# Kernel optimization log

Hardware: AMD Instinct MI355X
Metric: run time of the kernel (lower is better)

The kernel has to match this reference:

```python
import jax, jax.numpy as jnp
import numpy as np

V, E, D_LAT, NC, L = 30000, 256, 256, 10, 4096
B = 8
D_IN = 2 * D_LAT   # mamba expand=2 -> 512
N_ST = 16          # d_state
DT_R = 16          # dt_rank = ceil(d_model/16)
D_CONV = 4


def conv1d(x, w, b, pad, groups=1):
    # x: [B,C,L], w: [O, C//groups, K] (torch layout)
    y = jax.lax.conv_general_dilated(x, w, (1,), [(pad[0], pad[1])],
                                     dimension_numbers=('NCH', 'OIH', 'NCH'),
                                     feature_group_count=groups)
    return y + b[None, :, None]


def setup_inputs() -> dict:
    key = jax.random.key(0)
    ks = jax.random.split(key, 12)
    nrm = lambda k, s, sc=0.02: (jax.random.normal(k, s) * sc).astype(jnp.float32)
    return {
        'tokens': jax.random.randint(ks[0], (B, L), 0, V),
        'emb': nrm(ks[1], (V, E)),
        'conv1_w': nrm(ks[2], (128, E, 5)), 'conv1_b': jnp.zeros((128,), jnp.float32),
        'conv2_w': nrm(ks[3], (D_LAT, 128, 3)), 'conv2_b': jnp.zeros((D_LAT,), jnp.float32),
        'in_proj_w': nrm(ks[4], (2 * D_IN, D_LAT)),
        'convdw_w': nrm(ks[5], (D_IN, 1, D_CONV), 0.2), 'convdw_b': jnp.zeros((D_IN,), jnp.float32),
        'x_proj_w': nrm(ks[6], (DT_R + 2 * N_ST, D_IN)),
        'dt_proj_w': nrm(ks[7], (D_IN, DT_R), 0.1),
        'dt_proj_b': jnp.full((D_IN,), -4.0, jnp.float32),  # softplus^-1 of small dt
        'A_log': jnp.broadcast_to(jnp.log(jnp.arange(1, N_ST + 1, dtype=jnp.float32)), (D_IN, N_ST)) + jnp.zeros((D_IN, N_ST), jnp.float32),
        'Dp': jnp.ones((D_IN,), jnp.float32),
        'out_proj_w': nrm(ks[8], (D_LAT, D_IN)),
        'fc_w': nrm(ks[9], (NC, D_LAT)), 'fc_b': jnp.zeros((NC,), jnp.float32),
    }


def mamba_block(u, in_proj_w, convdw_w, convdw_b, x_proj_w, dt_proj_w, dt_proj_b, A_log, Dp, out_proj_w):
    # u: [B, Lm, d_model]
    Bsz = u.shape[0]
    xz = u @ in_proj_w.T                              # [B,Lm,2*Din]
    x, z = jnp.split(xz, 2, axis=-1)
    # causal depthwise conv (torch pads both sides, slices [:L] == left-pad only)
    xc = conv1d(x.transpose(0, 2, 1), convdw_w, convdw_b, (D_CONV - 1, 0), groups=D_IN)
    x = jax.nn.silu(xc.transpose(0, 2, 1))            # [B,Lm,Din]
    dbc = x @ x_proj_w.T                              # [B,Lm,dt_rank+2N]
    dt, Bm, Cm = jnp.split(dbc, [DT_R, DT_R + N_ST], axis=-1)
    dt = jax.nn.softplus(dt @ dt_proj_w.T + dt_proj_b)  # [B,Lm,Din]
    A = -jnp.exp(A_log)                               # [Din,N]

    def step(h, inp):
        dt_t, B_t, C_t, x_t = inp                     # [B,Din],[B,N],[B,N],[B,Din]
        dA = jnp.exp(dt_t[..., None] * A)             # [B,Din,N]
        h = h * dA + (dt_t * x_t)[..., None] * B_t[:, None, :]
        y = jnp.einsum('bdn,bn->bd', h, C_t)
        return h, y

    h0 = jnp.zeros((Bsz, D_IN, N_ST), u.dtype)
    xs = (dt.transpose(1, 0, 2), Bm.transpose(1, 0, 2), Cm.transpose(1, 0, 2), x.transpose(1, 0, 2))
    _, ys = jax.lax.scan(step, h0, xs)                # [Lm,B,Din]
    y = ys.transpose(1, 0, 2) + x * Dp
    y = y * jax.nn.silu(z)
    return y @ out_proj_w.T                           # [B,Lm,d_model]


def reference(tokens, emb, conv1_w, conv1_b, conv2_w, conv2_b, in_proj_w, convdw_w, convdw_b,
              x_proj_w, dt_proj_w, dt_proj_b, A_log, Dp, out_proj_w, fc_w, fc_b):
    x = emb[tokens]                                   # [B,L,E]
    x = x.transpose(0, 2, 1)                          # [B,E,L]
    x = jax.nn.relu(conv1d(x, conv1_w, conv1_b, (2, 2)))
    b, c, l = x.shape
    x = x.reshape(b, c, l // 2, 2).max(-1)            # MaxPool1d(2)
    x = jax.nn.relu(conv1d(x, conv2_w, conv2_b, (1, 1)))
    x = x.transpose(0, 2, 1)                          # [B,L/2,latent]
    x = mamba_block(x, in_proj_w, convdw_w, convdw_b, x_proj_w, dt_proj_w, dt_proj_b, A_log, Dp, out_proj_w)
    x = x.mean(axis=1)                                # [B,latent]
    return x @ fc_w.T + fc_b                          # [B,num_classes]
```

## Files before the change

### kernel.cpp

```cpp
#include <hip/hip_runtime.h>
#include <hip/hip_bf16.h>

constexpr int Bn   = 8;
constexpr int L    = 4096;
constexpr int E    = 256;
constexpr int Lh   = 2048;
constexpr int C1n  = 128;
constexpr int Dlat = 256;
constexpr int Din  = 512;
constexpr int Nst  = 16;
constexpr int M2   = Bn * Lh;
constexpr int NCH  = 64;
constexpr int TC   = 32;

constexpr long o_wtx   = 0;
constexpr long o_wtdt  = o_wtx  + 512L*48;
constexpr long o_bf    = o_wtdt + 16L*512;
constexpr long o_xeb   = o_bf    + 524288/2;
constexpr long o_out1b = o_xeb   + (8L*4100*256)/2;
constexpr long o_ub    = o_out1b + (8L*2050*128)/2;
constexpr long o_xz    = o_ub    + (16384L*256)/2;
constexpr long o_xbuf  = o_xz    + 16384L*1024;
constexpr long o_dbc   = o_xbuf  + 16384L*512;
constexpr long o_dt    = o_dbc   + 16384L*48;
constexpr long o_hend  = o_dt    + 16384L*512;
constexpr long o_P     = o_hend  + 8L*512*NCH*16;
constexpr long o_hin   = o_P     + 8L*512*NCH*16;
constexpr long o_ym    = o_hin   + 8L*512*NCH*16;
constexpr long o_S     = o_ym    + 8L*512;
constexpr long o_yp    = o_S     + 8L*512*NCH*16;

typedef __attribute__((ext_vector_type(8))) short bf8_t;
typedef __attribute__((ext_vector_type(4))) float f4_t;

__device__ inline short f2bf(float f) {
    unsigned int u = __float_as_uint(f);
    unsigned int r = (u + 0x7FFFu + ((u >> 16) & 1u)) >> 16;
    return (short)r;
}

__global__ void k_prep(const float* __restrict__ w1, const float* __restrict__ w2,
                       const float* __restrict__ win, const float* __restrict__ xw,
                       const float* __restrict__ dtw, float* __restrict__ ws) {
    int idx = blockIdx.x * 256 + threadIdx.x;
    if (idx < 24576) {
        int n_ = idx % 48; int k = idx / 48;
        ws[o_wtx + idx] = xw[n_*512 + k];
    } else if (idx < 32768) {
        int j = idx - 24576;
        int n_ = j & 511; int k = j >> 9;
        ws[o_wtdt + j] = dtw[n_*16 + k];
    } else if (idx < 557056) {
        int j = idx - 32768;
        short* wsS = (short*)(ws + o_bf);
        if (j < 163840) {
            int n_ = j / 1280; int r = j - n_*1280; int s = r >> 8; int c = r & 255;
            wsS[j] = f2bf(w1[(n_*256 + c)*5 + s]);
        } else if (j < 262144) {
            int jj = j - 163840;
            int n_ = jj / 384; int r = jj - n_*384; int s = r >> 7; int c = r & 127;
            wsS[j] = f2bf(w2[(n_*128 + c)*3 + s]);
        } else {
            int jj = j - 262144;
            int n_ = jj >> 8; int k = jj & 255;
            wsS[j] = f2bf(win[n_*256 + k]);
        }
    }
}

__global__ void k_embed(const int* __restrict__ tok, const float* __restrict__ emb,
                        short* __restrict__ xeb) {
    int idx = blockIdx.x * 256 + threadIdx.x;
    int r = idx >> 5;
    int c8 = (idx & 31) << 3;
    int b = r / 4100; int tr = r - b*4100;
    bf8_t v = {0,0,0,0,0,0,0,0};
    if (tr >= 2 && tr < 4098) {
        int t = tok[b*4096 + tr - 2];
        const float* e = emb + (long)t*256 + c8;
        #pragma unroll
        for (int i = 0; i < 8; ++i) v[i] = f2bf(e[i]);
    }
    *(bf8_t*)&xeb[(long)r*256 + c8] = v;
}

__global__ void k_zpad(short* __restrict__ out1b) {
    int i = threadIdx.x;
    for (int j = i; j < 2048; j += 256) {
        int b = j >> 8; int rsel = (j >> 7) & 1; int c = j & 127;
        long row = (long)b*2050 + (rsel ? 2049 : 0);
        out1b[row*128 + c] = 0;
    }
}

template<int SHIFTS, int TPS, int EPI>
__global__ __launch_bounds__(256) void k_mgemm(const short* __restrict__ A, int ars, long batchA,
                                               const short* __restrict__ Bt, int ktot,
                                               const float* __restrict__ bias,
                                               short* __restrict__ outB, float* __restrict__ outF,
                                               int ors, long batchOut) {
    constexpr int KT = SHIFTS * TPS;
    constexpr int C  = TPS * 64;
    __shared__ short As[2][64][68];
    __shared__ short Bs[2][128][68];
    int tid = threadIdx.x;
    int l = tid & 63, w = tid >> 6;
    int m0 = blockIdx.x * 64;
    int n0 = blockIdx.y * 128;
    long zA = (long)blockIdx.z * batchA;
    long zO = (long)blockIdx.z * batchOut;

    bf8_t aReg[2], bReg[4];

    auto gload = [&](int kt) {
        int s = kt / TPS, c0 = (kt % TPS) * 64;
        const short* Ab = A + zA + (long)(m0 + s) * ars + c0;
        #pragma unroll
        for (int j = 0; j < 2; ++j) {
            int idx = tid + j*256;
            int r = idx >> 3, cc = (idx & 7) * 8;
            aReg[j] = *(const bf8_t*)&Ab[(long)r * ars + cc];
        }
        const short* Bb = Bt + (long)n0 * ktot + s * C + c0;
        #pragma unroll
        for (int j = 0; j < 4; ++j) {
            int idx = tid + j*256;
            int r = idx >> 3, cc = (idx & 7) * 8;
            bReg[j] = *(const bf8_t*)&Bb[(long)r * ktot + cc];
        }
    };
    auto lwrite = [&](int buf) {
        #pragma unroll
        for (int j = 0; j < 2; ++j) {
            int idx = tid + j*256;
            int r = idx >> 3, cc = (idx & 7) * 8;
            *(bf8_t*)&As[buf][r][cc] = aReg[j];
        }
        #pragma unroll
        for (int j = 0; j < 4; ++j) {
            int idx = tid + j*256;
            int r = idx >> 3, cc = (idx & 7) * 8;
            *(bf8_t*)&Bs[buf][r][cc] = bReg[j];
        }
    };

    f4_t acc[4][2];
    #pragma unroll
    for (int m = 0; m < 4; ++m)
        #pragma unroll
        for (int n = 0; n < 2; ++n) acc[m][n] = (f4_t){0.f, 0.f, 0.f, 0.f};

    gload(0);
    lwrite(0);
    __syncthreads();
    for (int kt = 0; kt < KT; ++kt) {
        int buf = kt & 1;
        if (kt + 1 < KT) gload(kt + 1);
        #pragma unroll
        for (int ks = 0; ks < 2; ++ks) {
            int kk = ks*32 + ((l >> 4) << 3);
            bf8_t a[4], b[2];
            #pragma unroll
            for (int m = 0; m < 4; ++m)
                a[m] = *(const bf8_t*)&As[buf][m*16 + (l & 15)][kk];
            #pragma unroll
            for (int n = 0; n < 2; ++n)
                b[n] = *(const bf8_t*)&Bs[buf][w*32 + n*16 + (l & 15)][kk];
            #pragma unroll
            for (int m = 0; m < 4; ++m)
                #pragma unroll
                for (int n = 0; n < 2; ++n)
                    acc[m][n] = __builtin_amdgcn_mfma_f32_16x16x32_bf16(a[m], b[n], acc[m][n], 0, 0, 0);
        }
        if (kt + 1 < KT) {
            lwrite(buf ^ 1);
            __syncthreads();
        }
    }

    #pragma unroll
    for (int mt = 0; mt < 4; ++mt)
        #pragma unroll
        for (int nt = 0; nt < 2; ++nt) {
            f4_t c = acc[mt][nt];
            int col = n0 + w*32 + nt*16 + (l & 15);
            int r0 = m0 + mt*16 + ((l >> 4) << 2);
            if constexpr (EPI == 0) {
                #pragma unroll
                for (int j = 0; j < 4; ++j)
                    outF[zO + (long)(r0 + j) * ors + col] = c[j];
            } else if constexpr (EPI == 1) {
                float bv = bias[col];
                #pragma unroll
                for (int j = 0; j < 4; ++j)
                    outB[zO + (long)(r0 + j) * ors + col] = f2bf(fmaxf(c[j] + bv, 0.f));
            } else {
                float bv = bias[col];
                float p0 = fmaxf(fmaxf(c[0], c[1]) + bv, 0.f);
                float p1 = fmaxf(fmaxf(c[2], c[3]) + bv, 0.f);
                int tp = r0 >> 1;
                outB[zO + (long)(tp + 1) * ors + col] = f2bf(p0);
                outB[zO + (long)(tp + 2) * ors + col] = f2bf(p1);
            }
        }
}

template<int ACT>
__global__ __launch_bounds__(256) void k_gemm(const float* __restrict__ A, int lda,
                                              const float* __restrict__ WT,
                                              const float* __restrict__ bias,
                                              float* __restrict__ out,
                                              int M, int N, int K) {
    __shared__ float As[16][68];
    __shared__ float Bs[16][64];
    int n0 = blockIdx.x * 64, m0 = blockIdx.y * 64;
    int tid = threadIdx.x;
    int ti = tid >> 4, tj = tid & 15;
    float acc[4][4] = {};
    for (int k0 = 0; k0 < K; k0 += 16) {
        {
            int mm = tid >> 2, kq = tid & 3;
            float4 v = *(const float4*)&A[(long)(m0 + mm)*lda + k0 + kq*4];
            As[kq*4+0][mm] = v.x; As[kq*4+1][mm] = v.y;
            As[kq*4+2][mm] = v.z; As[kq*4+3][mm] = v.w;
        }
        {
            int kk = tid >> 4, n4 = tid & 15;
            float4 v = {0.f,0.f,0.f,0.f};
            if (n0 + n4*4 < N)
                v = *(const float4*)&WT[(long)(k0 + kk)*N + n0 + n4*4];
            *(float4*)&Bs[kk][n4*4] = v;
        }
        __syncthreads();
        #pragma unroll
        for (int kk = 0; kk < 16; ++kk) {
            float4 av = *(float4*)&As[kk][ti*4];
            float4 bv = *(float4*)&Bs[kk][tj*4];
            acc[0][0] += av.x*bv.x; acc[0][1] += av.x*bv.y; acc[0][2] += av.x*bv.z; acc[0][3] += av.x*bv.w;
            acc[1][0] += av.y*bv.x; acc[1][1] += av.y*bv.y; acc[1][2] += av.y*bv.z; acc[1][3] += av.y*bv.w;
            acc[2][0] += av.z*bv.x; acc[2][1] += av.z*bv.y; acc[2][2] += av.z*bv.z; acc[2][3] += av.z*bv.w;
            acc[3][0] += av.w*bv.x; acc[3][1] += av.w*bv.y; acc[3][2] += av.w*bv.z; acc[3][3] += av.w*bv.w;
        }
        __syncthreads();
    }
    if (n0 + tj*4 >= N) return;
    float4 bv = {0.f,0.f,0.f,0.f};
    if (bias) bv = *(const float4*)&bias[n0 + tj*4];
    #pragma unroll
    for (int i = 0; i < 4; ++i) {
        int m = m0 + ti*4 + i;
        float4 v;
        v.x = acc[i][0] + bv.x; v.y = acc[i][1] + bv.y;
        v.z = acc[i][2] + bv.z; v.w = acc[i][3] + bv.w;
        if (ACT == 1) {
            v.x = (v.x > 20.f) ? v.x : log1pf(__expf(v.x));
            v.y = (v.y > 20.f) ? v.y : log1pf(__expf(v.y));
            v.z = (v.z > 20.f) ? v.z : log1pf(__expf(v.z));
            v.w = (v.w > 20.f) ? v.w : log1pf(__expf(v.w));
        }
        *(float4*)&out[(long)m*N + n0 + tj*4] = v;
    }
}

__global__ __launch_bounds__(256) void k_dwconv(const float* __restrict__ xz,
                                                const float* __restrict__ wdw,
                                                const float* __restrict__ bdw,
                                                float* __restrict__ xout) {
    __shared__ float wk[4][512];
    __shared__ float bs[512];
    int tid = threadIdx.x;
    for (int e = tid; e < 2048; e += 256) {
        int k = e >> 9, d = e & 511;
        wk[k][d] = wdw[d*4 + k];
    }
    bs[tid] = bdw[tid];
    bs[tid + 256] = bdw[tid + 256];
    __syncthreads();

    int idx = blockIdx.x * 256 + tid;
    int d4 = idx & 127;
    int tg = (idx >> 7) & 511;
    int b  = idx >> 16;
    int d0 = d4 * 4;
    int t0 = tg * 4;

    float4 x[7];
    #pragma unroll
    for (int i = 0; i < 7; ++i) {
        int t = t0 - 3 + i;
        x[i] = (t >= 0) ? *(const float4*)&xz[((long)(b*Lh + t))*1024 + d0]
                        : (float4){0.f, 0.f, 0.f, 0.f};
    }
    float4 w[4];
    #pragma unroll
    for (int k = 0; k < 4; ++k) w[k] = *(float4*)&wk[k][d0];
    float4 bias4 = *(float4*)&bs[d0];

    #pragma unroll
    for (int j = 0; j < 4; ++j) {
        float4 a = bias4;
        #pragma unroll
        for (int k = 0; k < 4; ++k) {
            float4 v = x[j + k];
            a.x += v.x * w[k].x; a.y += v.y * w[k].y;
            a.z += v.z * w[k].z; a.w += v.w * w[k].w;
        }
        a.x = a.x / (1.f + __expf(-a.x));
        a.y = a.y / (1.f + __expf(-a.y));
        a.z = a.z / (1.f + __expf(-a.z));
        a.w = a.w / (1.f + __expf(-a.w));
        *(float4*)&xout[((long)(b*Lh + t0 + j))*512 + d0] = a;
    }
}

__global__ __launch_bounds__(256) void k_scan_a(const float* __restrict__ dt,
                                                const float* __restrict__ x,
                                                const float* __restrict__ xz,
                                                const float* __restrict__ dbc,
                                                const float* __restrict__ A_log,
                                                const float* __restrict__ Dp,
                                                float* __restrict__ hend,
                                                float* __restrict__ Pbuf,
                                                float* __restrict__ Sbuf,
                                                float* __restrict__ ypart) {
    __shared__ float4 Bs4[TC][4], Cs4[TC][4];
    int c = blockIdx.x;
    int b = blockIdx.z;
    int tid = threadIdx.x;
    int d = blockIdx.y * 256 + tid;
    for (int i = tid; i < TC*4; i += 256) {
        int tt = i >> 2, q = i & 3;
        long rb = ((long)b*Lh + c*TC + tt)*48;
        Bs4[tt][q] = *(const float4*)&dbc[rb + 16 + q*4];
        Cs4[tt][q] = *(const float4*)&dbc[rb + 32 + q*4];
    }
    __syncthreads();
    float A_[16];
    #pragma unroll
    for (int n = 0; n < 16; ++n) A_[n] = -__expf(A_log[d*16 + n]);
    float h[16], q[16], S[16];
    #pragma unroll
    for (int n = 0; n < 16; ++n) { h[n] = 0.f; q[n] = 1.f; S[n] = 0.f; }
    float Dpv = Dp[d];
    float yp = 0.f;
    long base  = ((long)b*Lh + c*TC)*512 + d;
    long zbase = ((long)b*Lh + c*TC)*1024 + 512 + d;
    for (int tt = 0; tt < TC; ++tt) {
        float dtv = dt[base + (long)tt*512];
        float xv  = x[base + (long)tt*512];
        float zv  = xz[zbase + (long)tt*1024];
        float u = dtv * xv;
        float gate = zv / (1.f + __expf(-zv));
        float Bv[16], Cv[16];
        *(float4*)&Bv[0]  = Bs4[tt][0]; *(float4*)&Bv[4]  = Bs4[tt][1];
        *(float4*)&Bv[8]  = Bs4[tt][2]; *(float4*)&Bv[12] = Bs4[tt][3];
        *(float4*)&Cv[0]  = Cs4[tt][0]; *(float4*)&Cv[4]  = Cs4[tt][1];
        *(float4*)&Cv[8]  = Cs4[tt][2]; *(float4*)&Cv[12] = Cs4[tt][3];
        float p = 0.f;
        #pragma unroll
        for (int n = 0; n < 16; ++n) {
            float dA = __expf(dtv * A_[n]);
            h[n] = h[n] * dA + u * Bv[n];
            q[n] *= dA;
            p += h[n] * Cv[n];
            S[n] += (gate * Cv[n]) * q[n];
        }
        yp += gate * (p + xv * Dpv);
    }
    long o = (((long)b*Din + d)*NCH + c)*16;
    #pragma unroll
    for (int n = 0; n < 16; ++n) hend[o + n] = h[n];
    #pragma unroll
    for (int n = 0; n < 16; ++n) Pbuf[o + n] = q[n];
    #pragma unroll
    for (int n = 0; n < 16; ++n) Sbuf[o + n] = S[n];
    ypart[((long)b*Din + d)*NCH + c] = yp;
}

__global__ void k_scan_b(const float* __restrict__ hend, const float* __restrict__ Pbuf,
                         float* __restrict__ hin) {
    int idx = blockIdx.x * 256 + threadIdx.x;
    int n = idx & 15; long bd = idx >> 4;
    long base = bd * NCH * 16 + n;
    float h = 0.f;
    for (int c = 0; c < NCH; ++c) {
        hin[base + c*16] = h;
        h = hend[base + c*16] + Pbuf[base + c*16] * h;
    }
}

__global__ __launch_bounds__(256) void k_scan_cl(const float* __restrict__ Sbuf,
                                                 const float* __restrict__ hin,
                                                 const float* __restrict__ ypart,
                                                 float* __restrict__ ym) {
    int idx = blockIdx.x * 256 + threadIdx.x;
    int c = idx & 63;
    long bd = idx >> 6;
    long o = (bd * NCH + c) * 16;
    float v = ypart[bd * NCH + c];
    #pragma unroll
    for (int qq = 0; qq < 4; ++qq) {
        float4 s = *(const float4*)&Sbuf[o + qq*4];
        float4 hi = *(const float4*)&hin[o + qq*4];
        v += s.x*hi.x + s.y*hi.y + s.z*hi.z + s.w*hi.w;
    }
    v += __shfl_xor(v, 1);
    v += __shfl_xor(v, 2);
    v += __shfl_xor(v, 4);
    v += __shfl_xor(v, 8);
    v += __shfl_xor(v, 16);
    v += __shfl_xor(v, 32);
    if (c == 0) ym[bd] = v;
}

__global__ void k_tail(const float* __restrict__ ym, const float* __restrict__ ow,
                       const float* __restrict__ fcw, const float* __restrict__ fcb,
                       float* __restrict__ out) {
    __shared__ float yls[512];
    __shared__ float xs[256];
    int b = blockIdx.x, c = threadIdx.x;
    yls[c] = ym[b*512 + c];
    yls[c + 256] = ym[b*512 + 256 + c];
    __syncthreads();
    float s = 0.f;
    for (int d = 0; d < 512; ++d) s += yls[d] * ow[c*512 + d];
    xs[c] = s * (1.f / 2048.f);
    __syncthreads();
    if (c < 10) {
        float t = fcb[c];
        for (int k = 0; k < 256; ++k) t += xs[k] * fcw[c*256 + k];
        out[b*10 + c] = t;
    }
}

extern "C" void kernel_launch(void* const* d_in, const int* in_sizes, int n_in,
                              void* d_out, int out_size, void* d_ws, size_t ws_size,
                              hipStream_t stream) {
    const int*   tok  = (const int*)d_in[0];
    const float* emb  = (const float*)d_in[1];
    const float* w1   = (const float*)d_in[2];
    const float* b1   = (const float*)d_in[3];
    const float* w2   = (const float*)d_in[4];
    const float* b2   = (const float*)d_in[5];
    const float* win  = (const float*)d_in[6];
    const float* wdw  = (const float*)d_in[7];
    const float* bdw  = (const float*)d_in[8];
    const float* xw   = (const float*)d_in[9];
    const float* dtw  = (const float*)d_in[10];
    const float* dtb  = (const float*)d_in[11];
    const float* alog = (const float*)d_in[12];
    const float* Dp   = (const float*)d_in[13];
    const float* ow   = (const float*)d_in[14];
    const float* fcw  = (const float*)d_in[15];
    const float* fcb  = (const float*)d_in[16];
    float* ws  = (float*)d_ws;
    float* out = (float*)d_out;

    float* wtx   = ws + o_wtx;
    float* wtdt  = ws + o_wtdt;
    short* wt1t  = (short*)(ws + o_bf);
    short* wt2t  = wt1t + 163840;
    short* wtint = wt2t + 98304;
    short* xeb   = (short*)(ws + o_xeb);
    short* out1b = (short*)(ws + o_out1b);
    short* ub    = (short*)(ws + o_ub);
    float* xz    = ws + o_xz;
    float* xbuf  = ws + o_xbuf;
    float* dbc   = ws + o_dbc;
    float* dtbuf = ws + o_dt;
    float* hend  = ws + o_hend;
    float* Pbuf  = ws + o_P;
    float* hin   = ws + o_hin;
    float* ym    = ws + o_ym;
    float* Sbuf  = ws + o_S;
    float* ypart = ws + o_yp;

    k_prep<<<2176, 256, 0, stream>>>(w1, w2, win, xw, dtw, ws);
    k_embed<<<4100, 256, 0, stream>>>(tok, emb, xeb);
    k_zpad<<<1, 256, 0, stream>>>(out1b);
    k_mgemm<5, 4, 2><<<dim3(64, 1, 8), 256, 0, stream>>>(
        xeb, 256, 4100L*256, wt1t, 1280, b1, out1b, nullptr, 128, 2050L*128);
    k_mgemm<3, 2, 1><<<dim3(32, 2, 8), 256, 0, stream>>>(
        out1b, 128, 2050L*128, wt2t, 384, b2, ub, nullptr, 256, 2048L*256);
    k_mgemm<1, 4, 0><<<dim3(256, 8, 1), 256, 0, stream>>>(
        ub, 256, 0, wtint, 256, nullptr, nullptr, xz, 1024, 0);
    k_dwconv<<<2048, 256, 0, stream>>>(xz, wdw, bdw, xbuf);
    k_gemm<0><<<dim3(1, M2/64), 256, 0, stream>>>(xbuf, Din, wtx, nullptr, dbc, M2, 48, Din);
    k_gemm<1><<<dim3(8, M2/64), 256, 0, stream>>>(dbc, 48, wtdt, dtb, dtbuf, M2, 512, 16);
    k_scan_a<<<dim3(NCH, 2, Bn), 256, 0, stream>>>(dtbuf, xbuf, xz, dbc, alog, Dp,
                                                   hend, Pbuf, Sbuf, ypart);
    k_scan_b<<<(Bn*Din*Nst)/256, 256, 0, stream>>>(hend, Pbuf, hin);
    k_scan_cl<<<(Bn*Din*NCH)/256, 256, 0, stream>>>(Sbuf, hin, ypart, ym);
    k_tail<<<8, 256, 0, stream>>>(ym, ow, fcw, fcb, out);
}
```

Before: 353.9 us.

## Fuse dt projection into scan, merge chunk-combine kernels, halve scan chunk length

Drops the separate dt_proj GEMM and its dt buffer. Each scan thread now computes dt from the 16 dt-rank values staged in shared memory, its own dt_proj weights, and softplus. The inter-chunk state recurrence and the S·h_in reduction are merged into one kernel, so the h_in buffer is no longer needed. Chunk count doubles to 128 with 16 steps each, which gives the scan more parallelism but makes the sequential combine loop and the chunk buffers twice as long.

```diff
diff --git a/kernel.cpp b/kernel.cpp
--- a/kernel.cpp
+++ b/kernel.cpp
@@ -10,8 +10,8 @@
 constexpr int Din  = 512;
 constexpr int Nst  = 16;
 constexpr int M2   = Bn * Lh;
-constexpr int NCH  = 64;
-constexpr int TC   = 32;
+constexpr int NCH  = 128;
+constexpr int TC   = 16;
 
 constexpr long o_wtx   = 0;
 constexpr long o_wtdt  = o_wtx  + 512L*48;
@@ -22,13 +22,11 @@
 constexpr long o_xz    = o_ub    + (16384L*256)/2;
 constexpr long o_xbuf  = o_xz    + 16384L*1024;
 constexpr long o_dbc   = o_xbuf  + 16384L*512;
-constexpr long o_dt    = o_dbc   + 16384L*48;
-constexpr long o_hend  = o_dt    + 16384L*512;
+constexpr long o_hend  = o_dbc   + 16384L*48;
 constexpr long o_P     = o_hend  + 8L*512*NCH*16;
-constexpr long o_hin   = o_P     + 8L*512*NCH*16;
-constexpr long o_ym    = o_hin   + 8L*512*NCH*16;
-constexpr long o_S     = o_ym    + 8L*512;
-constexpr long o_yp    = o_S     + 8L*512*NCH*16;
+constexpr long o_S     = o_P     + 8L*512*NCH*16;
+constexpr long o_ym    = o_S     + 8L*512*NCH*16;
+constexpr long o_yp    = o_ym    + 8L*512;
 
 typedef __attribute__((ext_vector_type(8))) short bf8_t;
 typedef __attribute__((ext_vector_type(4))) float f4_t;
@@ -313,31 +311,36 @@
     }
 }
 
-__global__ __launch_bounds__(256) void k_scan_a(const float* __restrict__ dt,
-                                                const float* __restrict__ x,
+__global__ __launch_bounds__(256) void k_scan_a(const float* __restrict__ x,
                                                 const float* __restrict__ xz,
                                                 const float* __restrict__ dbc,
+                                                const float* __restrict__ wtdt,
+                                                const float* __restrict__ dtb,
                                                 const float* __restrict__ A_log,
                                                 const float* __restrict__ Dp,
                                                 float* __restrict__ hend,
                                                 float* __restrict__ Pbuf,
                                                 float* __restrict__ Sbuf,
                                                 float* __restrict__ ypart) {
-    __shared__ float4 Bs4[TC][4], Cs4[TC][4];
+    __shared__ float4 Ds4[TC][4], Bs4[TC][4], Cs4[TC][4];
     int c = blockIdx.x;
     int b = blockIdx.z;
     int tid = threadIdx.x;
     int d = blockIdx.y * 256 + tid;
     for (int i = tid; i < TC*4; i += 256) {
-        int tt = i >> 2, q = i & 3;
+        int tt = i >> 2, qq = i & 3;
         long rb = ((long)b*Lh + c*TC + tt)*48;
-        Bs4[tt][q] = *(const float4*)&dbc[rb + 16 + q*4];
-        Cs4[tt][q] = *(const float4*)&dbc[rb + 32 + q*4];
+        Ds4[tt][qq] = *(const float4*)&dbc[rb + qq*4];
+        Bs4[tt][qq] = *(const float4*)&dbc[rb + 16 + qq*4];
+        Cs4[tt][qq] = *(const float4*)&dbc[rb + 32 + qq*4];
     }
     __syncthreads();
-    float A_[16];
+    float A_[16], wdt[16];
     #pragma unroll
     for (int n = 0; n < 16; ++n) A_[n] = -__expf(A_log[d*16 + n]);
+    #pragma unroll
+    for (int n = 0; n < 16; ++n) wdt[n] = wtdt[n*512 + d];
+    float dtbd = dtb[d];
     float h[16], q[16], S[16];
     #pragma unroll
     for (int n = 0; n < 16; ++n) { h[n] = 0.f; q[n] = 1.f; S[n] = 0.f; }
@@ -346,7 +349,13 @@
     long base  = ((long)b*Lh + c*TC)*512 + d;
     long zbase = ((long)b*Lh + c*TC)*1024 + 512 + d;
     for (int tt = 0; tt < TC; ++tt) {
-        float dtv = dt[base + (long)tt*512];
+        float dr[16];
+        *(float4*)&dr[0]  = Ds4[tt][0]; *(float4*)&dr[4]  = Ds4[tt][1];
+        *(float4*)&dr[8]  = Ds4[tt][2]; *(float4*)&dr[12] = Ds4[tt][3];
+        float raw = dtbd;
+        #pragma unroll
+        for (int k = 0; k < 16; ++k) raw += dr[k] * wdt[k];
+        float dtv = (raw > 20.f) ? raw : log1pf(__expf(raw));
         float xv  = x[base + (long)tt*512];
         float zv  = xz[zbase + (long)tt*1024];
         float u = dtv * xv;
@@ -377,40 +386,28 @@
     ypart[((long)b*Din + d)*NCH + c] = yp;
 }
 
-__global__ void k_scan_b(const float* __restrict__ hend, const float* __restrict__ Pbuf,
-                         float* __restrict__ hin) {
+__global__ __launch_bounds__(256) void k_scan_bc(const float* __restrict__ hend,
+                                                 const float* __restrict__ Pbuf,
+                                                 const float* __restrict__ Sbuf,
+                                                 const float* __restrict__ ypart,
+                                                 float* __restrict__ ym) {
     int idx = blockIdx.x * 256 + threadIdx.x;
     int n = idx & 15; long bd = idx >> 4;
     long base = bd * NCH * 16 + n;
-    float h = 0.f;
+    float h = 0.f, acc = 0.f;
     for (int c = 0; c < NCH; ++c) {
-        hin[base + c*16] = h;
-        h = hend[base + c*16] + Pbuf[base + c*16] * h;
-    }
-}
-
-__global__ __launch_bounds__(256) void k_scan_cl(const float* __restrict__ Sbuf,
-                                                 const float* __restrict__ hin,
-                                                 const float* __restrict__ ypart,
-                                                 float* __restrict__ ym) {
-    int idx = blockIdx.x * 256 + threadIdx.x;
-    int c = idx & 63;
-    long bd = idx >> 6;
-    long o = (bd * NCH + c) * 16;
-    float v = ypart[bd * NCH + c];
-    #pragma unroll
-    for (int qq = 0; qq < 4; ++qq) {
-        float4 s = *(const float4*)&Sbuf[o + qq*4];
-        float4 hi = *(const float4*)&hin[o + qq*4];
-        v += s.x*hi.x + s.y*hi.y + s.z*hi.z + s.w*hi.w;
-    }
-    v += __shfl_xor(v, 1);
-    v += __shfl_xor(v, 2);
-    v += __shfl_xor(v, 4);
-    v += __shfl_xor(v, 8);
-    v += __shfl_xor(v, 16);
-    v += __shfl_xor(v, 32);
-    if (c == 0) ym[bd] = v;
+        long o = base + (long)c*16;
+        acc += Sbuf[o] * h;
+        h = hend[o] + Pbuf[o] * h;
+    }
+    #pragma unroll
+    for (int k = 0; k < 8; ++k)
+        acc += ypart[bd * NCH + n + k*16];
+    acc += __shfl_xor(acc, 1);
+    acc += __shfl_xor(acc, 2);
+    acc += __shfl_xor(acc, 4);
+    acc += __shfl_xor(acc, 8);
+    if (n == 0) ym[bd] = acc;
 }
 
 __global__ void k_tail(const float* __restrict__ ym, const float* __restrict__ ow,
@@ -467,12 +464,10 @@
     float* xz    = ws + o_xz;
     float* xbuf  = ws + o_xbuf;
     float* dbc   = ws + o_dbc;
-    float* dtbuf = ws + o_dt;
     float* hend  = ws + o_hend;
     float* Pbuf  = ws + o_P;
-    float* hin   = ws + o_hin;
+    float* Sbuf  = ws + o_S;
     float* ym    = ws + o_ym;
-    float* Sbuf  = ws + o_S;
     float* ypart = ws + o_yp;
 
     k_prep<<<2176, 256, 0, stream>>>(w1, w2, win, xw, dtw, ws);
@@ -486,10 +481,8 @@
         ub, 256, 0, wtint, 256, nullptr, nullptr, xz, 1024, 0);
     k_dwconv<<<2048, 256, 0, stream>>>(xz, wdw, bdw, xbuf);
     k_gemm<0><<<dim3(1, M2/64), 256, 0, stream>>>(xbuf, Din, wtx, nullptr, dbc, M2, 48, Din);
-    k_gemm<1><<<dim3(8, M2/64), 256, 0, stream>>>(dbc, 48, wtdt, dtb, dtbuf, M2, 512, 16);
-    k_scan_a<<<dim3(NCH, 2, Bn), 256, 0, stream>>>(dtbuf, xbuf, xz, dbc, alog, Dp,
+    k_scan_a<<<dim3(NCH, 2, Bn), 256, 0, stream>>>(xbuf, xz, dbc, wtdt, dtb, alog, Dp,
                                                    hend, Pbuf, Sbuf, ypart);
-    k_scan_b<<<(Bn*Din*Nst)/256, 256, 0, stream>>>(hend, Pbuf, hin);
-    k_scan_cl<<<(Bn*Din*NCH)/256, 256, 0, stream>>>(Sbuf, hin, ypart, ym);
+    k_scan_bc<<<(Bn*Din*Nst)/256, 256, 0, stream>>>(hend, Pbuf, Sbuf, ypart, ym);
     k_tail<<<8, 256, 0, stream>>>(ym, ow, fcw, fcb, out);
 }
```

New measurement: 344.5 us. 1.03x faster.
